# Kernel tuning notes

Measured on AMD Instinct MI355X. Metric: run time of the kernel, lower is better.

## Reference

```python
import jax, jax.numpy as jnp
import numpy as np

NUM_DAYS = 4096
NUM_ATTR = 512
MB = 128  # minibatch_size (sliding-window length)
HID = 500


def setup_inputs() -> dict:
    key = jax.random.key(0)
    kx, k1, kb1, k2, kb2 = jax.random.split(key, 5)
    bound1 = 1.0 / np.sqrt(NUM_ATTR)
    bound2 = 1.0 / np.sqrt(HID)
    return {
        "x": jax.random.normal(kx, (NUM_DAYS, NUM_ATTR), dtype=jnp.float32),
        "W1": jax.random.uniform(k1, (NUM_ATTR, HID), jnp.float32, -bound1, bound1),
        "b1": jax.random.uniform(kb1, (HID,), jnp.float32, -bound1, bound1),
        "W2": jax.random.uniform(k2, (HID, 1), jnp.float32, -bound2, bound2),
        "b2": jax.random.uniform(kb2, (1,), jnp.float32, -bound2, bound2),
    }


def reference(x, W1, b1, W2, b2):
    num_days = x.shape[0]
    num_batches = num_days - MB  # number of sliding windows
    # window gather indices: [num_batches, MB]
    idx = jnp.arange(num_batches)[:, None] + jnp.arange(MB)[None, :]
    xw = x[idx]                                   # [num_batches, MB, num_attr]
    h = jnp.einsum('wma,ah->wmh', xw, W1) + b1    # [num_batches, MB, 500]
    out = jnp.einsum('wmh,ho->wmo', h, W2) + b2   # [num_batches, MB, 1]
    # torch loop cats all windows along dim 0 (first window replaces sentinel)
    return out.reshape(num_batches * MB, 1)
```

## Files before the change

### kernel.cpp

```cpp
#include <hip/hip_runtime.h>

#define NUM_DAYS    4096
#define NUM_ATTR    512
#define MB_WIN      128
#define HID         500
#define NUM_BATCHES (NUM_DAYS - MB_WIN)
#define NUM_Y       (NUM_BATCHES + MB_WIN - 1)
#define OUT_ELEMS   (NUM_BATCHES * MB_WIN)

__global__ __launch_bounds__(64) void k_fold_weights(
    const float* __restrict__ W1, const float* __restrict__ b1,
    const float* __restrict__ W2, const float* __restrict__ b2,
    float* __restrict__ v, float* __restrict__ c) {
    const int b    = blockIdx.x;
    const int lane = threadIdx.x;
    const float* src = (b < NUM_ATTR) ? (W1 + (size_t)b * HID) : b1;
    float acc = 0.f;
    const float4* s4 = (const float4*)src;
    const float4* w4 = (const float4*)W2;
    #pragma unroll
    for (int j = lane; j < 125; j += 64) {
        float4 a = s4[j], w = w4[j];
        acc += a.x * w.x + a.y * w.y + a.z * w.z + a.w * w.w;
    }
    #pragma unroll
    for (int off = 32; off >= 1; off >>= 1) acc += __shfl_down(acc, off, 64);
    if (lane == 0) {
        if (b < NUM_ATTR) v[b] = acc;
        else              *c   = acc + b2[0];
    }
}

__global__ __launch_bounds__(256) void k_dot(
    const float* __restrict__ x, const float* __restrict__ v,
    const float* __restrict__ c, float* __restrict__ y) {
    const int wv   = threadIdx.x >> 6;
    const int lane = threadIdx.x & 63;
    const int d    = (blockIdx.x << 2) | wv;
    if (d >= NUM_Y) return;

    const float4* xr = (const float4*)(x + (size_t)d * NUM_ATTR);
    const float4* vr = (const float4*)v;
    float4 a0 = xr[lane];
    float4 a1 = xr[lane + 64];
    float4 v0 = vr[lane];
    float4 v1 = vr[lane + 64];
    float acc = a0.x * v0.x + a0.y * v0.y + a0.z * v0.z + a0.w * v0.w
              + a1.x * v1.x + a1.y * v1.y + a1.z * v1.z + a1.w * v1.w;
    #pragma unroll
    for (int off = 32; off >= 1; off >>= 1) acc += __shfl_xor(acc, off, 64);
    if (lane == 0) y[d] = acc + *c;
}

__global__ __launch_bounds__(256) void k_replicate(
    const float* __restrict__ y, float4* __restrict__ out4) {
    const int t = blockIdx.x * 256 + threadIdx.x;
    const int w = t >> 5;
    const int l = t & 31;
    const int base = w + (l << 2);
    float4 r;
    r.x = y[base + 0];
    r.y = y[base + 1];
    r.z = y[base + 2];
    r.w = y[base + 3];
    out4[t] = r;
}

extern "C" void kernel_launch(void* const* d_in, const int* in_sizes, int n_in,
                              void* d_out, int out_size, void* d_ws, size_t ws_size,
                              hipStream_t stream) {
    const float* x  = (const float*)d_in[0];
    const float* W1 = (const float*)d_in[1];
    const float* b1 = (const float*)d_in[2];
    const float* W2 = (const float*)d_in[3];
    const float* b2 = (const float*)d_in[4];
    float* out = (float*)d_out;

    float* ws = (float*)d_ws;
    float* v  = ws;
    float* c  = ws + 512;
    float* y  = ws + 576;

    k_fold_weights<<<NUM_ATTR + 1, 64, 0, stream>>>(W1, b1, W2, b2, v, c);
    k_dot<<<(NUM_Y + 3) / 4, 256, 0, stream>>>(x, v, c, y);
    k_replicate<<<(OUT_ELEMS / 4) / 256, 256, 0, stream>>>(y, (float4*)out);
}
```

Measured before the change: 68.40 us.

## Fuse weight-fold, dot and replicate kernels into one cooperative kernel

Replaces the three separate launches (fold W1·W2, per-row dot with x, replicate into sliding-window output) with a single cooperative kernel of 1024 blocks that separates the phases with grid-wide syncs. The aim is to remove the launch gaps and inter-kernel drain between the three small stages. In exchange it adds two grid barriers and depends on all 1024 blocks being co-resident, which the launch bound of 4 blocks per CU is meant to allow.

```diff
diff --git a/kernel.cpp b/kernel.cpp
--- a/kernel.cpp
+++ b/kernel.cpp
@@ -1,4 +1,7 @@
 #include <hip/hip_runtime.h>
+#include <hip/hip_cooperative_groups.h>
+
+namespace cg = cooperative_groups;
 
 #define NUM_DAYS    4096
 #define NUM_ATTR    512
@@ -8,62 +11,65 @@
 #define NUM_Y       (NUM_BATCHES + MB_WIN - 1)
 #define OUT_ELEMS   (NUM_BATCHES * MB_WIN)
 
-__global__ __launch_bounds__(64) void k_fold_weights(
-    const float* __restrict__ W1, const float* __restrict__ b1,
-    const float* __restrict__ W2, const float* __restrict__ b2,
-    float* __restrict__ v, float* __restrict__ c) {
-    const int b    = blockIdx.x;
-    const int lane = threadIdx.x;
-    const float* src = (b < NUM_ATTR) ? (W1 + (size_t)b * HID) : b1;
-    float acc = 0.f;
-    const float4* s4 = (const float4*)src;
-    const float4* w4 = (const float4*)W2;
-    #pragma unroll
-    for (int j = lane; j < 125; j += 64) {
-        float4 a = s4[j], w = w4[j];
-        acc += a.x * w.x + a.y * w.y + a.z * w.z + a.w * w.w;
+__global__ __launch_bounds__(256, 4) void k_fused(
+    const float* __restrict__ x,  const float* __restrict__ W1,
+    const float* __restrict__ b1, const float* __restrict__ W2,
+    const float* __restrict__ b2, float* __restrict__ v,
+    float* __restrict__ c,        float* __restrict__ y,
+    float4* __restrict__ out4)
+{
+    cg::grid_group grid = cg::this_grid();
+    const int tid  = blockIdx.x * 256 + threadIdx.x;
+    const int g    = tid >> 6;
+    const int lane = tid & 63;
+
+    if (g <= NUM_ATTR) {
+        const float* src = (g < NUM_ATTR) ? (W1 + (size_t)g * HID) : b1;
+        const float4* s4 = (const float4*)src;
+        const float4* w4 = (const float4*)W2;
+        float acc = 0.f;
+        #pragma unroll
+        for (int j = lane; j < 125; j += 64) {
+            float4 a = s4[j], w = w4[j];
+            acc += a.x * w.x + a.y * w.y + a.z * w.z + a.w * w.w;
+        }
+        #pragma unroll
+        for (int off = 32; off >= 1; off >>= 1) acc += __shfl_down(acc, off, 64);
+        if (lane == 0) {
+            if (g < NUM_ATTR) v[g] = acc;
+            else              *c   = acc + b2[0];
+        }
     }
-    #pragma unroll
-    for (int off = 32; off >= 1; off >>= 1) acc += __shfl_down(acc, off, 64);
-    if (lane == 0) {
-        if (b < NUM_ATTR) v[b] = acc;
-        else              *c   = acc + b2[0];
+
+    grid.sync();
+
+    if (g < NUM_Y) {
+        const float4* xr = (const float4*)(x + (size_t)g * NUM_ATTR);
+        const float4* vr = (const float4*)v;
+        float4 a0 = xr[lane];
+        float4 a1 = xr[lane + 64];
+        float4 v0 = vr[lane];
+        float4 v1 = vr[lane + 64];
+        float acc = a0.x * v0.x + a0.y * v0.y + a0.z * v0.z + a0.w * v0.w
+                  + a1.x * v1.x + a1.y * v1.y + a1.z * v1.z + a1.w * v1.w;
+        #pragma unroll
+        for (int off = 32; off >= 1; off >>= 1) acc += __shfl_xor(acc, off, 64);
+        if (lane == 0) y[g] = acc + *c;
     }
-}
 
-__global__ __launch_bounds__(256) void k_dot(
-    const float* __restrict__ x, const float* __restrict__ v,
-    const float* __restrict__ c, float* __restrict__ y) {
-    const int wv   = threadIdx.x >> 6;
-    const int lane = threadIdx.x & 63;
-    const int d    = (blockIdx.x << 2) | wv;
-    if (d >= NUM_Y) return;
+    grid.sync();
 
-    const float4* xr = (const float4*)(x + (size_t)d * NUM_ATTR);
-    const float4* vr = (const float4*)v;
-    float4 a0 = xr[lane];
-    float4 a1 = xr[lane + 64];
-    float4 v0 = vr[lane];
-    float4 v1 = vr[lane + 64];
-    float acc = a0.x * v0.x + a0.y * v0.y + a0.z * v0.z + a0.w * v0.w
-              + a1.x * v1.x + a1.y * v1.y + a1.z * v1.z + a1.w * v1.w;
-    #pragma unroll
-    for (int off = 32; off >= 1; off >>= 1) acc += __shfl_xor(acc, off, 64);
-    if (lane == 0) y[d] = acc + *c;
-}
-
-__global__ __launch_bounds__(256) void k_replicate(
-    const float* __restrict__ y, float4* __restrict__ out4) {
-    const int t = blockIdx.x * 256 + threadIdx.x;
-    const int w = t >> 5;
-    const int l = t & 31;
-    const int base = w + (l << 2);
-    float4 r;
-    r.x = y[base + 0];
-    r.y = y[base + 1];
-    r.z = y[base + 2];
-    r.w = y[base + 3];
-    out4[t] = r;
+    if (tid < OUT_ELEMS / 4) {
+        const int w    = tid >> 5;
+        const int l    = tid & 31;
+        const int base = w + (l << 2);
+        float4 r;
+        r.x = y[base + 0];
+        r.y = y[base + 1];
+        r.z = y[base + 2];
+        r.w = y[base + 3];
+        out4[tid] = r;
+    }
 }
 
 extern "C" void kernel_launch(void* const* d_in, const int* in_sizes, int n_in,
@@ -74,14 +80,15 @@
     const float* b1 = (const float*)d_in[2];
     const float* W2 = (const float*)d_in[3];
     const float* b2 = (const float*)d_in[4];
-    float* out = (float*)d_out;
+    float4* out = (float4*)d_out;
 
     float* ws = (float*)d_ws;
     float* v  = ws;
     float* c  = ws + 512;
     float* y  = ws + 576;
 
-    k_fold_weights<<<NUM_ATTR + 1, 64, 0, stream>>>(W1, b1, W2, b2, v, c);
-    k_dot<<<(NUM_Y + 3) / 4, 256, 0, stream>>>(x, v, c, y);
-    k_replicate<<<(OUT_ELEMS / 4) / 256, 256, 0, stream>>>(y, (float4*)out);
+    void* args[] = { (void*)&x, (void*)&W1, (void*)&b1, (void*)&W2, (void*)&b2,
+                     (void*)&v, (void*)&c,  (void*)&y,  (void*)&out };
+    hipLaunchCooperativeKernel((const void*)k_fused,
+                               dim3(1024), dim3(256), args, 0, stream);
 }
```

Result: slower. 237.5 us (+247.3%).
